# Optimization experiments

Hardware: AMD Instinct MI355X
Metric: run time of the kernel (lower is better)

The kernel has to match this reference:

```python
import jax, jax.numpy as jnp
import numpy as np

NUM_HEADS = 12   # H
NUM_TASKS = 4    # T
TOP_K = 2        # capacity_factor


def setup_inputs() -> dict:
    key = jax.random.key(0)
    ks = jax.random.split(key, 4)
    B, N, C = 2, 4100, 768  # N = NUM_TASKS + M, M = 4096
    x = jax.random.normal(ks[0], (B, N, C), dtype=jnp.float32)
    # torch.nn.Linear weights are [out_features, in_features]; y = x @ W.T
    qs_w = jax.random.normal(ks[1], (NUM_TASKS, C, C), dtype=jnp.float32) * 0.02
    kv_w = jax.random.normal(ks[2], (2 * C, C), dtype=jnp.float32) * 0.02
    experts_w = jax.random.normal(ks[3], (NUM_TASKS, C, C), dtype=jnp.float32) * 0.02
    return {"x": x, "qs_w": qs_w, "kv_w": kv_w, "experts_w": experts_w}


def reference(x, qs_w, kv_w, experts_w):
    B, N, C = x.shape
    T, H, K = NUM_TASKS, NUM_HEADS, TOP_K
    d = C // H
    M = N - T
    scale = d ** -0.5

    feature = x[:, T:, :]                                    # [B,M,C]
    kv = (feature @ kv_w.T).reshape(B, M, 2, H, d)
    k = jnp.transpose(kv[:, :, 0], (0, 2, 1, 3))             # [B,H,M,d]
    v = jnp.transpose(kv[:, :, 1], (0, 2, 1, 3))             # [B,H,M,d]

    # per-task q projections on task tokens (qs_w[t] is [out,in])
    q = jnp.einsum('btc,toc->bto', x[:, :T], qs_w)           # [B,T,C]
    q = q.reshape(B, T, H, d).transpose(0, 2, 1, 3)          # [B,H,T,d]

    attn = jnp.einsum('bhtd,bhmd->bhtm', q, k) * scale       # [B,H,T,M]
    topv, topi = jax.lax.top_k(attn, K)                      # [B,H,T,K]
    topw = jax.nn.softmax(topv, axis=-1)                     # softmax over top-k only

    # scatter softmaxed top-k back into dense [B,H,T,M] (indices unique per row)
    oh = jax.nn.one_hot(topi, M, dtype=x.dtype)              # [B,H,T,K,M]
    attn_topk = jnp.einsum('bhtk,bhtkm->bhtm', topw, oh)
    attn_token = jnp.einsum('bhtm,bhmd->bhtd', attn_topk, v)
    attn_token = attn_token.transpose(0, 2, 1, 3).reshape(B, T, C)   # [B,T,C]

    # gather top-k feature rows per head/task, weight, and scatter back
    fm = feature.reshape(B, M, H, d).transpose(0, 2, 1, 3)   # [B,H,M,d]
    feat_topk = jnp.take_along_axis(fm[:, :, None], topi[..., None], axis=3)  # [B,H,T,K,d]
    feat_topk = feat_topk * topw[..., None]
    # scatter to [B,H,T,M,d], then permute(0,2,3,1,4)+reshape -> [B,T,M,C]
    feat_pad = jnp.einsum('bhtkd,bhtkm->btmhd', feat_topk, oh).reshape(B, T, M, C)

    # per-task experts (no bias); einsum('btnc,btnc->bnc') with ones = sum over t
    feature_output = jnp.einsum('btmc,toc->bmo', feat_pad, experts_w)  # [B,M,C]
    token_output = jnp.einsum('btc,toc->bto', attn_token, experts_w)   # [B,T,C]

    return jnp.concatenate([token_output, feature_output], axis=1)     # [B,N,C]
```

## Files before the change

### kernel.cpp

```cpp
#include <hip/hip_runtime.h>
#include <math.h>

#define B_ 2
#define N_ 4100
#define C_ 768
#define T_ 4
#define H_ 12
#define D_ 64
#define M_ 4096
#define S_ 48
#define KS_ 12
#define KC_ 64
#define SCALE 0.125f

__device__ __forceinline__ bool better(float va, int ia, float vb, int ib) {
  return (va > vb) || (va == vb && ia < ib);
}

__device__ __forceinline__ void merge2(float& v1, int& i1, float& v2, int& i2,
                                       float ov1, int oi1, float ov2, int oi2) {
  if (better(ov1, oi1, v1, i1)) {
    float tv; int ti;
    tv = v1; ti = i1; v1 = ov1; i1 = oi1; ov1 = tv; oi1 = ti;
    tv = v2; ti = i2; v2 = ov2; i2 = oi2; ov2 = tv; oi2 = ti;
  }
  if (better(ov1, oi1, v2, i2)) { v2 = ov1; i2 = oi1; }
}

__global__ __launch_bounds__(256) void qk_kernel(const float* __restrict__ x,
    const float* __restrict__ qs_w, const float* __restrict__ kv_w,
    float* __restrict__ qk) {
  const int h = blockIdx.x % H_;
  const int t = (blockIdx.x / H_) % T_;
  const int b = blockIdx.x / S_;
  const int tid = threadIdx.x;
  __shared__ float xs[C_];
  __shared__ float red[256];
  __shared__ float qseg[D_];
  for (int i = tid; i < C_; i += 256) xs[i] = x[((size_t)b * N_ + t) * C_ + i];
  __syncthreads();
  {
    const int j = tid & 63;
    const int pt = tid >> 6;
    const float* wr = qs_w + ((size_t)t * C_ + h * D_ + j) * C_ + pt * 192;
    float a = 0.f;
    for (int c = 0; c < 192; ++c) a += xs[pt * 192 + c] * wr[c];
    red[tid] = a;
  }
  __syncthreads();
  if (tid < 64)
    qseg[tid] = (red[tid] + red[tid + 64] + red[tid + 128] + red[tid + 192]) * SCALE;
  __syncthreads();
  for (int c = tid; c < C_; c += 256) {
    float a = 0.f;
    #pragma unroll 8
    for (int j = 0; j < 64; ++j) a += qseg[j] * kv_w[((size_t)(h * D_ + j)) * C_ + c];
    qk[((size_t)blockIdx.x) * C_ + c] = a;
  }
}

__global__ __launch_bounds__(256) void score_kernel(const float* __restrict__ x,
    const float* __restrict__ qk, float* __restrict__ part) {
  const int mt = blockIdx.x & 63;
  const int b = blockIdx.x >> 6;
  const int kc = blockIdx.y;
  const int tid = threadIdx.x;
  const int m0 = mt * 64;

  __shared__ __align__(16) float fbuf[64][68];
  __shared__ __align__(16) float qkbuf[48][68];

  const float* xb = x + ((size_t)b * N_ + T_ + m0) * C_ + kc * KC_;
  const float* qkb = qk + (size_t)b * S_ * C_ + kc * KC_;

  for (int i = tid; i < 64 * 16; i += 256) {
    int row = i >> 4, c4 = i & 15;
    *(float4*)&fbuf[row][c4 * 4] =
        *(const float4*)(xb + (size_t)row * C_ + c4 * 4);
  }
  for (int i = tid; i < 48 * 16; i += 256) {
    int s = i >> 4, c4 = i & 15;
    *(float4*)&qkbuf[s][c4 * 4] =
        *(const float4*)(qkb + (size_t)s * C_ + c4 * 4);
  }
  __syncthreads();

  const int mg = tid & 15;
  const int sg = tid >> 4;

  float acc[4][3];
  #pragma unroll
  for (int u = 0; u < 4; ++u)
    #pragma unroll
    for (int i = 0; i < 3; ++i) acc[u][i] = 0.f;

  #pragma unroll 4
  for (int c4 = 0; c4 < 16; ++c4) {
    float4 f[4], q[3];
    f[0] = *(const float4*)&fbuf[mg][c4 * 4];
    f[1] = *(const float4*)&fbuf[mg + 16][c4 * 4];
    f[2] = *(const float4*)&fbuf[mg + 32][c4 * 4];
    f[3] = *(const float4*)&fbuf[mg + 48][c4 * 4];
    q[0] = *(const float4*)&qkbuf[sg * 3 + 0][c4 * 4];
    q[1] = *(const float4*)&qkbuf[sg * 3 + 1][c4 * 4];
    q[2] = *(const float4*)&qkbuf[sg * 3 + 2][c4 * 4];
    #pragma unroll
    for (int u = 0; u < 4; ++u)
      #pragma unroll
      for (int i = 0; i < 3; ++i)
        acc[u][i] += f[u].x * q[i].x + f[u].y * q[i].y +
                     f[u].z * q[i].z + f[u].w * q[i].w;
  }

  #pragma unroll
  for (int i = 0; i < 3; ++i) {
    int s = sg * 3 + i;
    float* pp = part + (((size_t)kc * B_ + b) * S_ + s) * M_ + m0 + mg;
    #pragma unroll
    for (int u = 0; u < 4; ++u) pp[16 * u] = acc[u][i];
  }
}

__global__ __launch_bounds__(256) void gather_kernel(const float* __restrict__ x,
    const float* __restrict__ kv_w, const float* __restrict__ experts_w,
    const float* __restrict__ part, float* __restrict__ out) {
  const int h = blockIdx.x % H_;
  const int t = (blockIdx.x / H_) % T_;
  const int b = blockIdx.x / S_;
  const int tid = threadIdx.x;

  __shared__ float f0[C_], f1[C_], fc[C_], red[256];
  __shared__ float attnh[D_];
  __shared__ float cbuf[4][4];
  __shared__ float sel[4];

  {
    float v1 = -INFINITY, v2 = -INFINITY;
    int i1 = 0x7fffffff, i2 = 0x7fffffff;
    const float* p0 = part + ((size_t)b * S_ + (t * H_ + h)) * M_;
    const size_t kstride = (size_t)B_ * S_ * M_;
    for (int m = tid; m < M_; m += 256) {
      float v = 0.f;
      #pragma unroll
      for (int kc = 0; kc < KS_; ++kc) v += p0[kc * kstride + m];
      if (better(v, m, v1, i1)) { v2 = v1; i2 = i1; v1 = v; i1 = m; }
      else if (better(v, m, v2, i2)) { v2 = v; i2 = m; }
    }
    #pragma unroll
    for (int off = 1; off < 64; off <<= 1) {
      float ov1 = __shfl_xor(v1, off);
      int   oi1 = __shfl_xor(i1, off);
      float ov2 = __shfl_xor(v2, off);
      int   oi2 = __shfl_xor(i2, off);
      merge2(v1, i1, v2, i2, ov1, oi1, ov2, oi2);
    }
    const int w = tid >> 6, lane = tid & 63;
    if (lane == 0) {
      cbuf[w][0] = v1; ((int*)cbuf[w])[1] = i1;
      cbuf[w][2] = v2; ((int*)cbuf[w])[3] = i2;
    }
    __syncthreads();
    if (tid == 0) {
      for (int ww = 1; ww < 4; ++ww)
        merge2(v1, i1, v2, i2, cbuf[ww][0], ((int*)cbuf[ww])[1],
               cbuf[ww][2], ((int*)cbuf[ww])[3]);
      float w1 = 1.f / (1.f + expf(v2 - v1));
      ((int*)sel)[0] = i1; ((int*)sel)[1] = i2;
      sel[2] = w1; sel[3] = 1.f - w1;
    }
    __syncthreads();
  }
  const int i1 = ((const int*)sel)[0];
  const int i2 = ((const int*)sel)[1];
  const float w1 = sel[2], w2 = sel[3];

  const float* r0 = x + ((size_t)b * N_ + T_ + i1) * C_;
  const float* r1 = x + ((size_t)b * N_ + T_ + i2) * C_;
  for (int i = tid; i < C_; i += 256) {
    float a = r0[i], bb = r1[i];
    f0[i] = a; f1[i] = bb; fc[i] = w1 * a + w2 * bb;
  }
  __syncthreads();

  const int j = tid & 63, pt = tid >> 6;
  {
    const float* kr = kv_w + ((size_t)(C_ + h * D_ + j)) * C_ + pt * 192;
    float a = 0.f;
    for (int c = 0; c < 192; ++c) a += fc[pt * 192 + c] * kr[c];
    red[tid] = a;
  }
  __syncthreads();
  if (tid < 64)
    attnh[tid] = red[tid] + red[tid + 64] + red[tid + 128] + red[tid + 192];
  __syncthreads();

  const size_t ot = ((size_t)b * N_ + t) * C_;
  const size_t o0 = ((size_t)b * N_ + T_ + i1) * C_;
  const size_t o1 = ((size_t)b * N_ + T_ + i2) * C_;
  for (int o = tid; o < C_; o += 256) {
    const float* er = experts_w + ((size_t)t * C_ + o) * C_ + h * D_;
    float at = 0.f, a0 = 0.f, a1 = 0.f;
    #pragma unroll 8
    for (int c = 0; c < D_; ++c) {
      float e = er[c];
      at += e * attnh[c];
      a0 += e * f0[h * D_ + c];
      a1 += e * f1[h * D_ + c];
    }
    atomicAdd(&out[ot + o], at);
    atomicAdd(&out[o0 + o], w1 * a0);
    atomicAdd(&out[o1 + o], w2 * a1);
  }
}

extern "C" void kernel_launch(void* const* d_in, const int* in_sizes, int n_in,
                              void* d_out, int out_size, void* d_ws, size_t ws_size,
                              hipStream_t stream) {
  const float* x         = (const float*)d_in[0];
  const float* qs_w      = (const float*)d_in[1];
  const float* kv_w      = (const float*)d_in[2];
  const float* experts_w = (const float*)d_in[3];
  float* out = (float*)d_out;

  float* ws   = (float*)d_ws;
  float* qk   = ws;
  float* part = qk + (size_t)B_ * S_ * C_;

  hipMemsetAsync(d_out, 0, (size_t)out_size * sizeof(float), stream);

  hipLaunchKernelGGL(qk_kernel,    dim3(B_ * S_),      dim3(256), 0, stream, x, qs_w, kv_w, qk);
  hipLaunchKernelGGL(score_kernel, dim3(B_ * 64, KS_), dim3(256), 0, stream, x, qk, part);
  hipLaunchKernelGGL(gather_kernel,dim3(B_ * S_),      dim3(256), 0, stream, x, kv_w, experts_w, part, out);
}
```

Before: 153.3 us.

## Split top-2 reduction into separate wide kernel and fold output zeroing into kernels

Moves the split-K partial-score summation and top-2 selection out of the 96-block gather kernel into a new reduce kernel with 768 blocks. Each block emits a candidate pair, and the gather kernel merges the 8 candidates per row. The output memset is replaced by zero writes inside qk_kernel (task rows) and score_kernel (feature rows), which removes a separate memset launch. The cost is one extra kernel launch plus a small candidate buffer in workspace.

```diff
diff --git a/kernel.cpp b/kernel.cpp
--- a/kernel.cpp
+++ b/kernel.cpp
@@ -11,6 +11,7 @@
 #define S_ 48
 #define KS_ 12
 #define KC_ 64
+#define SEG_ 8
 #define SCALE 0.125f
 
 __device__ __forceinline__ bool better(float va, int ia, float vb, int ib) {
@@ -29,7 +30,7 @@
 
 __global__ __launch_bounds__(256) void qk_kernel(const float* __restrict__ x,
     const float* __restrict__ qs_w, const float* __restrict__ kv_w,
-    float* __restrict__ qk) {
+    float* __restrict__ qk, float* __restrict__ out) {
   const int h = blockIdx.x % H_;
   const int t = (blockIdx.x / H_) % T_;
   const int b = blockIdx.x / S_;
@@ -37,6 +38,8 @@
   __shared__ float xs[C_];
   __shared__ float red[256];
   __shared__ float qseg[D_];
+  if (h == 0)
+    for (int i = tid; i < C_; i += 256) out[((size_t)b * N_ + t) * C_ + i] = 0.f;
   for (int i = tid; i < C_; i += 256) xs[i] = x[((size_t)b * N_ + t) * C_ + i];
   __syncthreads();
   {
@@ -60,7 +63,7 @@
 }
 
 __global__ __launch_bounds__(256) void score_kernel(const float* __restrict__ x,
-    const float* __restrict__ qk, float* __restrict__ part) {
+    const float* __restrict__ qk, float* __restrict__ part, float* __restrict__ out) {
   const int mt = blockIdx.x & 63;
   const int b = blockIdx.x >> 6;
   const int kc = blockIdx.y;
@@ -69,6 +72,12 @@
 
   __shared__ __align__(16) float fbuf[64][68];
   __shared__ __align__(16) float qkbuf[48][68];
+
+  if (kc == 0) {
+    float4 z = make_float4(0.f, 0.f, 0.f, 0.f);
+    float4* outv = (float4*)(out + ((size_t)b * N_ + T_ + m0) * C_);
+    for (int i = tid; i < 64 * C_ / 4; i += 256) outv[i] = z;
+  }
 
   const float* xb = x + ((size_t)b * N_ + T_ + m0) * C_ + kc * KC_;
   const float* qkb = qk + (size_t)b * S_ * C_ + kc * KC_;
@@ -121,9 +130,50 @@
   }
 }
 
+__global__ __launch_bounds__(256) void reduce_kernel(const float* __restrict__ part,
+                                                     float* __restrict__ cand) {
+  const int seg = blockIdx.x & 7;
+  const int bs = blockIdx.x >> 3;
+  const int tid = threadIdx.x;
+  const size_t kstride = (size_t)B_ * S_ * M_;
+  const float* p0 = part + (size_t)bs * M_ + seg * 512 + tid * 2;
+  float a0 = 0.f, a1 = 0.f;
+  #pragma unroll
+  for (int kc = 0; kc < KS_; ++kc) {
+    float2 v = *(const float2*)(p0 + kc * kstride);
+    a0 += v.x; a1 += v.y;
+  }
+  const int mA = seg * 512 + tid * 2;
+  float v1, v2; int i1, i2;
+  if (better(a0, mA, a1, mA + 1)) { v1 = a0; i1 = mA; v2 = a1; i2 = mA + 1; }
+  else                            { v1 = a1; i1 = mA + 1; v2 = a0; i2 = mA; }
+  #pragma unroll
+  for (int off = 1; off < 64; off <<= 1) {
+    float ov1 = __shfl_xor(v1, off);
+    int   oi1 = __shfl_xor(i1, off);
+    float ov2 = __shfl_xor(v2, off);
+    int   oi2 = __shfl_xor(i2, off);
+    merge2(v1, i1, v2, i2, ov1, oi1, ov2, oi2);
+  }
+  __shared__ float cbuf[4][4];
+  const int w = tid >> 6, lane = tid & 63;
+  if (lane == 0) {
+    cbuf[w][0] = v1; ((int*)cbuf[w])[1] = i1;
+    cbuf[w][2] = v2; ((int*)cbuf[w])[3] = i2;
+  }
+  __syncthreads();
+  if (tid == 0) {
+    for (int ww = 1; ww < 4; ++ww)
+      merge2(v1, i1, v2, i2, cbuf[ww][0], ((int*)cbuf[ww])[1],
+             cbuf[ww][2], ((int*)cbuf[ww])[3]);
+    ((float4*)cand)[blockIdx.x] =
+        make_float4(v1, __int_as_float(i1), v2, __int_as_float(i2));
+  }
+}
+
 __global__ __launch_bounds__(256) void gather_kernel(const float* __restrict__ x,
     const float* __restrict__ kv_w, const float* __restrict__ experts_w,
-    const float* __restrict__ part, float* __restrict__ out) {
+    const float* __restrict__ cand, float* __restrict__ out) {
   const int h = blockIdx.x % H_;
   const int t = (blockIdx.x / H_) % T_;
   const int b = blockIdx.x / S_;
@@ -131,45 +181,27 @@
 
   __shared__ float f0[C_], f1[C_], fc[C_], red[256];
   __shared__ float attnh[D_];
-  __shared__ float cbuf[4][4];
   __shared__ float sel[4];
 
-  {
-    float v1 = -INFINITY, v2 = -INFINITY;
-    int i1 = 0x7fffffff, i2 = 0x7fffffff;
-    const float* p0 = part + ((size_t)b * S_ + (t * H_ + h)) * M_;
-    const size_t kstride = (size_t)B_ * S_ * M_;
-    for (int m = tid; m < M_; m += 256) {
-      float v = 0.f;
-      #pragma unroll
-      for (int kc = 0; kc < KS_; ++kc) v += p0[kc * kstride + m];
-      if (better(v, m, v1, i1)) { v2 = v1; i2 = i1; v1 = v; i1 = m; }
-      else if (better(v, m, v2, i2)) { v2 = v; i2 = m; }
-    }
-    #pragma unroll
-    for (int off = 1; off < 64; off <<= 1) {
+  if (tid < 8) {
+    float4 cv = ((const float4*)cand)[blockIdx.x * 8 + tid];
+    float v1 = cv.x, v2 = cv.z;
+    int i1 = __float_as_int(cv.y), i2 = __float_as_int(cv.w);
+    #pragma unroll
+    for (int off = 1; off < 8; off <<= 1) {
       float ov1 = __shfl_xor(v1, off);
       int   oi1 = __shfl_xor(i1, off);
       float ov2 = __shfl_xor(v2, off);
       int   oi2 = __shfl_xor(i2, off);
       merge2(v1, i1, v2, i2, ov1, oi1, ov2, oi2);
     }
-    const int w = tid >> 6, lane = tid & 63;
-    if (lane == 0) {
-      cbuf[w][0] = v1; ((int*)cbuf[w])[1] = i1;
-      cbuf[w][2] = v2; ((int*)cbuf[w])[3] = i2;
-    }
-    __syncthreads();
     if (tid == 0) {
-      for (int ww = 1; ww < 4; ++ww)
-        merge2(v1, i1, v2, i2, cbuf[ww][0], ((int*)cbuf[ww])[1],
-               cbuf[ww][2], ((int*)cbuf[ww])[3]);
       float w1 = 1.f / (1.f + expf(v2 - v1));
       ((int*)sel)[0] = i1; ((int*)sel)[1] = i2;
       sel[2] = w1; sel[3] = 1.f - w1;
     }
-    __syncthreads();
-  }
+  }
+  __syncthreads();
   const int i1 = ((const int*)sel)[0];
   const int i2 = ((const int*)sel)[1];
   const float w1 = sel[2], w2 = sel[3];
@@ -225,10 +257,10 @@
   float* ws   = (float*)d_ws;
   float* qk   = ws;
   float* part = qk + (size_t)B_ * S_ * C_;
-
-  hipMemsetAsync(d_out, 0, (size_t)out_size * sizeof(float), stream);
-
-  hipLaunchKernelGGL(qk_kernel,    dim3(B_ * S_),      dim3(256), 0, stream, x, qs_w, kv_w, qk);
-  hipLaunchKernelGGL(score_kernel, dim3(B_ * 64, KS_), dim3(256), 0, stream, x, qk, part);
-  hipLaunchKernelGGL(gather_kernel,dim3(B_ * S_),      dim3(256), 0, stream, x, kv_w, experts_w, part, out);
-}
+  float* cand = part + (size_t)KS_ * B_ * S_ * M_;
+
+  hipLaunchKernelGGL(qk_kernel,     dim3(B_ * S_),        dim3(256), 0, stream, x, qs_w, kv_w, qk, out);
+  hipLaunchKernelGGL(score_kernel,  dim3(B_ * 64, KS_),   dim3(256), 0, stream, x, qk, part, out);
+  hipLaunchKernelGGL(reduce_kernel, dim3(B_ * S_ * SEG_), dim3(256), 0, stream, part, cand);
+  hipLaunchKernelGGL(gather_kernel, dim3(B_ * S_),        dim3(256), 0, stream, x, kv_w, experts_w, cand, out);
+}
```

Result: faster. 149.7 us (-2.3%).

## Fuse score and gather into a cooperative kernel and fold output zeroing into qk

Applied to the files above, without the earlier changes.

Merges the score and gather kernels into one cooperative launch separated by a grid-wide sync. The output memset now runs inside spare blocks of the q-projection kernel, so there are fewer launches and no separate memset. The K-split drops from 12 to 6 chunks of 128 channels, which halves the partial-score traffic the gather reads, and the gather's partial reduction now uses float4 loads. The cost is a grid barrier with 768 blocks that must all be co-resident. A fallback path with two separate launches handles the case where the cooperative launch fails.

```diff
diff --git a/kernel.cpp b/kernel.cpp
--- a/kernel.cpp
+++ b/kernel.cpp
@@ -1,5 +1,8 @@
 #include <hip/hip_runtime.h>
+#include <hip/hip_cooperative_groups.h>
 #include <math.h>
+
+namespace cg = cooperative_groups;
 
 #define B_ 2
 #define N_ 4100
@@ -9,8 +12,9 @@
 #define D_ 64
 #define M_ 4096
 #define S_ 48
-#define KS_ 12
-#define KC_ 64
+#define KS_ 6
+#define KC_ 128
+#define GRID_ 768
 #define SCALE 0.125f
 
 __device__ __forceinline__ bool better(float va, int ia, float vb, int ib) {
@@ -27,89 +31,97 @@
   if (better(ov1, oi1, v2, i2)) { v2 = ov1; i2 = oi1; }
 }
 
-__global__ __launch_bounds__(256) void qk_kernel(const float* __restrict__ x,
+__global__ __launch_bounds__(256) void qkzero_kernel(const float* __restrict__ x,
     const float* __restrict__ qs_w, const float* __restrict__ kv_w,
-    float* __restrict__ qk) {
-  const int h = blockIdx.x % H_;
-  const int t = (blockIdx.x / H_) % T_;
-  const int b = blockIdx.x / S_;
+    float* __restrict__ qk, float* __restrict__ out) {
+  const int blk = blockIdx.x;
   const int tid = threadIdx.x;
-  __shared__ float xs[C_];
-  __shared__ float red[256];
-  __shared__ float qseg[D_];
-  for (int i = tid; i < C_; i += 256) xs[i] = x[((size_t)b * N_ + t) * C_ + i];
-  __syncthreads();
-  {
-    const int j = tid & 63;
-    const int pt = tid >> 6;
-    const float* wr = qs_w + ((size_t)t * C_ + h * D_ + j) * C_ + pt * 192;
-    float a = 0.f;
-    for (int c = 0; c < 192; ++c) a += xs[pt * 192 + c] * wr[c];
-    red[tid] = a;
-  }
-  __syncthreads();
-  if (tid < 64)
-    qseg[tid] = (red[tid] + red[tid + 64] + red[tid + 128] + red[tid + 192]) * SCALE;
-  __syncthreads();
-  for (int c = tid; c < C_; c += 256) {
-    float a = 0.f;
-    #pragma unroll 8
-    for (int j = 0; j < 64; ++j) a += qseg[j] * kv_w[((size_t)(h * D_ + j)) * C_ + c];
-    qk[((size_t)blockIdx.x) * C_ + c] = a;
-  }
-}
-
-__global__ __launch_bounds__(256) void score_kernel(const float* __restrict__ x,
-    const float* __restrict__ qk, float* __restrict__ part) {
-  const int mt = blockIdx.x & 63;
-  const int b = blockIdx.x >> 6;
-  const int kc = blockIdx.y;
-  const int tid = threadIdx.x;
+  if (blk < B_ * S_) {
+    const int h = blk % H_;
+    const int t = (blk / H_) % T_;
+    const int b = blk / S_;
+    __shared__ float xs[C_];
+    __shared__ float red[256];
+    __shared__ float qseg[D_];
+    for (int i = tid; i < C_; i += 256) xs[i] = x[((size_t)b * N_ + t) * C_ + i];
+    __syncthreads();
+    {
+      const int j = tid & 63;
+      const int pt = tid >> 6;
+      const float* wr = qs_w + ((size_t)t * C_ + h * D_ + j) * C_ + pt * 192;
+      float a = 0.f;
+      for (int c = 0; c < 192; ++c) a += xs[pt * 192 + c] * wr[c];
+      red[tid] = a;
+    }
+    __syncthreads();
+    if (tid < 64)
+      qseg[tid] = (red[tid] + red[tid + 64] + red[tid + 128] + red[tid + 192]) * SCALE;
+    __syncthreads();
+    for (int c = tid; c < C_; c += 256) {
+      float a = 0.f;
+      #pragma unroll 8
+      for (int j = 0; j < 64; ++j) a += qseg[j] * kv_w[((size_t)(h * D_ + j)) * C_ + c];
+      qk[(size_t)blk * C_ + c] = a;
+    }
+  } else {
+    const int zb = blk - B_ * S_;
+    const int NV4 = (B_ * N_ * C_) / 4;
+    float4 z = make_float4(0.f, 0.f, 0.f, 0.f);
+    float4* ov = (float4*)out;
+    for (int i = zb * 256 + tid; i < NV4; i += (GRID_ - B_ * S_) * 256) ov[i] = z;
+  }
+}
+
+__device__ __forceinline__ void score_body(int blk, int tid, const float* __restrict__ x,
+    const float* __restrict__ qk, float* __restrict__ part, float* smem) {
+  const int mt = blk & 63;
+  const int b = (blk >> 6) & 1;
+  const int kc = blk >> 7;
   const int m0 = mt * 64;
-
-  __shared__ __align__(16) float fbuf[64][68];
-  __shared__ __align__(16) float qkbuf[48][68];
+  float (*fbuf)[68] = (float(*)[68])smem;
+  float (*qkbuf)[68] = (float(*)[68])(smem + 64 * 68);
+  const int mg = tid & 15;
+  const int sg = tid >> 4;
+
+  float acc[4][3];
+  #pragma unroll
+  for (int u = 0; u < 4; ++u)
+    #pragma unroll
+    for (int i = 0; i < 3; ++i) acc[u][i] = 0.f;
 
   const float* xb = x + ((size_t)b * N_ + T_ + m0) * C_ + kc * KC_;
   const float* qkb = qk + (size_t)b * S_ * C_ + kc * KC_;
 
-  for (int i = tid; i < 64 * 16; i += 256) {
-    int row = i >> 4, c4 = i & 15;
-    *(float4*)&fbuf[row][c4 * 4] =
-        *(const float4*)(xb + (size_t)row * C_ + c4 * 4);
-  }
-  for (int i = tid; i < 48 * 16; i += 256) {
-    int s = i >> 4, c4 = i & 15;
-    *(float4*)&qkbuf[s][c4 * 4] =
-        *(const float4*)(qkb + (size_t)s * C_ + c4 * 4);
-  }
-  __syncthreads();
-
-  const int mg = tid & 15;
-  const int sg = tid >> 4;
-
-  float acc[4][3];
-  #pragma unroll
-  for (int u = 0; u < 4; ++u)
-    #pragma unroll
-    for (int i = 0; i < 3; ++i) acc[u][i] = 0.f;
-
-  #pragma unroll 4
-  for (int c4 = 0; c4 < 16; ++c4) {
-    float4 f[4], q[3];
-    f[0] = *(const float4*)&fbuf[mg][c4 * 4];
-    f[1] = *(const float4*)&fbuf[mg + 16][c4 * 4];
-    f[2] = *(const float4*)&fbuf[mg + 32][c4 * 4];
-    f[3] = *(const float4*)&fbuf[mg + 48][c4 * 4];
-    q[0] = *(const float4*)&qkbuf[sg * 3 + 0][c4 * 4];
-    q[1] = *(const float4*)&qkbuf[sg * 3 + 1][c4 * 4];
-    q[2] = *(const float4*)&qkbuf[sg * 3 + 2][c4 * 4];
-    #pragma unroll
-    for (int u = 0; u < 4; ++u)
+  for (int cc = 0; cc < KC_ / 64; ++cc) {
+    __syncthreads();
+    for (int i = tid; i < 64 * 16; i += 256) {
+      int row = i >> 4, c4 = i & 15;
+      *(float4*)&fbuf[row][c4 * 4] =
+          *(const float4*)(xb + (size_t)row * C_ + cc * 64 + c4 * 4);
+    }
+    for (int i = tid; i < 48 * 16; i += 256) {
+      int s = i >> 4, c4 = i & 15;
+      *(float4*)&qkbuf[s][c4 * 4] =
+          *(const float4*)(qkb + (size_t)s * C_ + cc * 64 + c4 * 4);
+    }
+    __syncthreads();
+    #pragma unroll 4
+    for (int c4 = 0; c4 < 16; ++c4) {
+      float4 f[4], q[3];
+      f[0] = *(const float4*)&fbuf[mg][c4 * 4];
+      f[1] = *(const float4*)&fbuf[mg + 16][c4 * 4];
+      f[2] = *(const float4*)&fbuf[mg + 32][c4 * 4];
+      f[3] = *(const float4*)&fbuf[mg + 48][c4 * 4];
+      q[0] = *(const float4*)&qkbuf[sg * 3 + 0][c4 * 4];
+      q[1] = *(const float4*)&qkbuf[sg * 3 + 1][c4 * 4];
+      q[2] = *(const float4*)&qkbuf[sg * 3 + 2][c4 * 4];
       #pragma unroll
-      for (int i = 0; i < 3; ++i)
-        acc[u][i] += f[u].x * q[i].x + f[u].y * q[i].y +
-                     f[u].z * q[i].z + f[u].w * q[i].w;
+      for (int u = 0; u < 4; ++u)
+        #pragma unroll
+        for (int i = 0; i < 3; ++i)
+          acc[u][i] += f[u].x * q[i].x + f[u].y * q[i].y +
+                       f[u].z * q[i].z + f[u].w * q[i].w;
+    }
   }
 
   #pragma unroll
@@ -121,61 +133,70 @@
   }
 }
 
-__global__ __launch_bounds__(256) void gather_kernel(const float* __restrict__ x,
+__device__ __forceinline__ void gather_body(int blk, int tid, const float* __restrict__ x,
     const float* __restrict__ kv_w, const float* __restrict__ experts_w,
-    const float* __restrict__ part, float* __restrict__ out) {
-  const int h = blockIdx.x % H_;
-  const int t = (blockIdx.x / H_) % T_;
-  const int b = blockIdx.x / S_;
-  const int tid = threadIdx.x;
-
-  __shared__ float f0[C_], f1[C_], fc[C_], red[256];
-  __shared__ float attnh[D_];
-  __shared__ float cbuf[4][4];
-  __shared__ float sel[4];
-
-  {
-    float v1 = -INFINITY, v2 = -INFINITY;
-    int i1 = 0x7fffffff, i2 = 0x7fffffff;
-    const float* p0 = part + ((size_t)b * S_ + (t * H_ + h)) * M_;
-    const size_t kstride = (size_t)B_ * S_ * M_;
-    for (int m = tid; m < M_; m += 256) {
-      float v = 0.f;
-      #pragma unroll
-      for (int kc = 0; kc < KS_; ++kc) v += p0[kc * kstride + m];
-      if (better(v, m, v1, i1)) { v2 = v1; i2 = i1; v1 = v; i1 = m; }
-      else if (better(v, m, v2, i2)) { v2 = v; i2 = m; }
-    }
-    #pragma unroll
-    for (int off = 1; off < 64; off <<= 1) {
-      float ov1 = __shfl_xor(v1, off);
-      int   oi1 = __shfl_xor(i1, off);
-      float ov2 = __shfl_xor(v2, off);
-      int   oi2 = __shfl_xor(i2, off);
-      merge2(v1, i1, v2, i2, ov1, oi1, ov2, oi2);
-    }
-    const int w = tid >> 6, lane = tid & 63;
-    if (lane == 0) {
-      cbuf[w][0] = v1; ((int*)cbuf[w])[1] = i1;
-      cbuf[w][2] = v2; ((int*)cbuf[w])[3] = i2;
-    }
-    __syncthreads();
-    if (tid == 0) {
-      for (int ww = 1; ww < 4; ++ww)
-        merge2(v1, i1, v2, i2, cbuf[ww][0], ((int*)cbuf[ww])[1],
-               cbuf[ww][2], ((int*)cbuf[ww])[3]);
-      float w1 = 1.f / (1.f + expf(v2 - v1));
-      ((int*)sel)[0] = i1; ((int*)sel)[1] = i2;
-      sel[2] = w1; sel[3] = 1.f - w1;
-    }
-    __syncthreads();
-  }
-  const int i1 = ((const int*)sel)[0];
-  const int i2 = ((const int*)sel)[1];
+    const float* __restrict__ part, float* __restrict__ out, float* smem) {
+  const int h = blk % H_;
+  const int t = (blk / H_) % T_;
+  const int b = blk / S_;
+  float* f0 = smem;
+  float* f1 = smem + 768;
+  float* fc = smem + 1536;
+  float* red = smem + 2304;
+  float* attnh = smem + 2560;
+  float* sel = smem + 2624;
+  float (*cbuf)[4] = (float(*)[4])(smem + 2640);
+  __syncthreads();
+
+  float v1 = -INFINITY, v2 = -INFINITY;
+  int i1 = 0x7fffffff, i2 = 0x7fffffff;
+  const float* p0 = part + (size_t)blk * M_;
+  const size_t kstride = (size_t)B_ * S_ * M_;
+  #pragma unroll
+  for (int ii = 0; ii < 4; ++ii) {
+    const int m = ii * 1024 + tid * 4;
+    float4 a = make_float4(0.f, 0.f, 0.f, 0.f);
+    #pragma unroll
+    for (int kc = 0; kc < KS_; ++kc) {
+      float4 v = *(const float4*)(p0 + kc * kstride + m);
+      a.x += v.x; a.y += v.y; a.z += v.z; a.w += v.w;
+    }
+    const float av[4] = {a.x, a.y, a.z, a.w};
+    #pragma unroll
+    for (int c = 0; c < 4; ++c) {
+      if (better(av[c], m + c, v1, i1)) { v2 = v1; i2 = i1; v1 = av[c]; i1 = m + c; }
+      else if (better(av[c], m + c, v2, i2)) { v2 = av[c]; i2 = m + c; }
+    }
+  }
+  #pragma unroll
+  for (int off = 1; off < 64; off <<= 1) {
+    float ov1 = __shfl_xor(v1, off);
+    int   oi1 = __shfl_xor(i1, off);
+    float ov2 = __shfl_xor(v2, off);
+    int   oi2 = __shfl_xor(i2, off);
+    merge2(v1, i1, v2, i2, ov1, oi1, ov2, oi2);
+  }
+  const int w = tid >> 6, lane = tid & 63;
+  if (lane == 0) {
+    cbuf[w][0] = v1; ((int*)cbuf[w])[1] = i1;
+    cbuf[w][2] = v2; ((int*)cbuf[w])[3] = i2;
+  }
+  __syncthreads();
+  if (tid == 0) {
+    for (int ww = 1; ww < 4; ++ww)
+      merge2(v1, i1, v2, i2, cbuf[ww][0], ((int*)cbuf[ww])[1],
+             cbuf[ww][2], ((int*)cbuf[ww])[3]);
+    float w1 = 1.f / (1.f + expf(v2 - v1));
+    ((int*)sel)[0] = i1; ((int*)sel)[1] = i2;
+    sel[2] = w1; sel[3] = 1.f - w1;
+  }
+  __syncthreads();
+  const int s1 = ((const int*)sel)[0];
+  const int s2 = ((const int*)sel)[1];
   const float w1 = sel[2], w2 = sel[3];
 
-  const float* r0 = x + ((size_t)b * N_ + T_ + i1) * C_;
-  const float* r1 = x + ((size_t)b * N_ + T_ + i2) * C_;
+  const float* r0 = x + ((size_t)b * N_ + T_ + s1) * C_;
+  const float* r1 = x + ((size_t)b * N_ + T_ + s2) * C_;
   for (int i = tid; i < C_; i += 256) {
     float a = r0[i], bb = r1[i];
     f0[i] = a; f1[i] = bb; fc[i] = w1 * a + w2 * bb;
@@ -195,8 +216,8 @@
   __syncthreads();
 
   const size_t ot = ((size_t)b * N_ + t) * C_;
-  const size_t o0 = ((size_t)b * N_ + T_ + i1) * C_;
-  const size_t o1 = ((size_t)b * N_ + T_ + i2) * C_;
+  const size_t o0 = ((size_t)b * N_ + T_ + s1) * C_;
+  const size_t o1 = ((size_t)b * N_ + T_ + s2) * C_;
   for (int o = tid; o < C_; o += 256) {
     const float* er = experts_w + ((size_t)t * C_ + o) * C_ + h * D_;
     float at = 0.f, a0 = 0.f, a1 = 0.f;
@@ -213,6 +234,32 @@
   }
 }
 
+__global__ __launch_bounds__(256) void coop_kernel(const float* __restrict__ x,
+    const float* __restrict__ kv_w, const float* __restrict__ experts_w,
+    const float* __restrict__ qk, float* __restrict__ part, float* __restrict__ out) {
+  cg::grid_group grid = cg::this_grid();
+  __shared__ __align__(16) float smem[7616];
+  score_body(blockIdx.x, threadIdx.x, x, qk, part, smem);
+  __threadfence();
+  grid.sync();
+  __threadfence();
+  if (blockIdx.x < B_ * S_)
+    gather_body(blockIdx.x, threadIdx.x, x, kv_w, experts_w, part, out, smem);
+}
+
+__global__ __launch_bounds__(256) void score_only(const float* __restrict__ x,
+    const float* __restrict__ qk, float* __restrict__ part) {
+  __shared__ __align__(16) float smem[7616];
+  score_body(blockIdx.x, threadIdx.x, x, qk, part, smem);
+}
+
+__global__ __launch_bounds__(256) void gather_only(const float* __restrict__ x,
+    const float* __restrict__ kv_w, const float* __restrict__ experts_w,
+    const float* __restrict__ part, float* __restrict__ out) {
+  __shared__ __align__(16) float smem[7616];
+  gather_body(blockIdx.x, threadIdx.x, x, kv_w, experts_w, part, out, smem);
+}
+
 extern "C" void kernel_launch(void* const* d_in, const int* in_sizes, int n_in,
                               void* d_out, int out_size, void* d_ws, size_t ws_size,
                               hipStream_t stream) {
@@ -222,13 +269,20 @@
   const float* experts_w = (const float*)d_in[3];
   float* out = (float*)d_out;
 
-  float* ws   = (float*)d_ws;
-  float* qk   = ws;
+  float* qk   = (float*)d_ws;
   float* part = qk + (size_t)B_ * S_ * C_;
 
-  hipMemsetAsync(d_out, 0, (size_t)out_size * sizeof(float), stream);
-
-  hipLaunchKernelGGL(qk_kernel,    dim3(B_ * S_),      dim3(256), 0, stream, x, qs_w, kv_w, qk);
-  hipLaunchKernelGGL(score_kernel, dim3(B_ * 64, KS_), dim3(256), 0, stream, x, qk, part);
-  hipLaunchKernelGGL(gather_kernel,dim3(B_ * S_),      dim3(256), 0, stream, x, kv_w, experts_w, part, out);
-}
+  hipLaunchKernelGGL(qkzero_kernel, dim3(GRID_), dim3(256), 0, stream,
+                     x, qs_w, kv_w, qk, out);
+
+  void* args[] = {(void*)&x, (void*)&kv_w, (void*)&experts_w,
+                  (void*)&qk, (void*)&part, (void*)&out};
+  hipError_t err = hipLaunchCooperativeKernel(
+      reinterpret_cast<void*>(coop_kernel), dim3(GRID_), dim3(256), args, 0, stream);
+  if (err != hipSuccess) {
+    (void)hipGetLastError();
+    hipLaunchKernelGGL(score_only,  dim3(GRID_),   dim3(256), 0, stream, x, qk, part);
+    hipLaunchKernelGGL(gather_only, dim3(B_ * S_), dim3(256), 0, stream,
+                       x, kv_w, experts_w, part, out);
+  }
+}
```

Result: slower. 350.3 us (+128.5%).
